# Kernel optimization log

Hardware: AMD Instinct MI355X
Metric: run time of the kernel (lower is better)

## Reference

```python
import jax, jax.numpy as jnp
import numpy as np

SL = 10   # seq_len hard-coded in rearrange
H = 20    # hidden size hard-coded in nn.LSTM
I = 128   # input_size
B = 32768 # batch


def setup_inputs() -> dict:
    key = jax.random.key(0)
    ks = jax.random.split(key, 9)
    k = 1.0 / np.sqrt(H)  # PyTorch LSTM init range
    u = lambda kk, shp: jax.random.uniform(kk, shp, jnp.float32, -k, k)
    return {
        "x": jax.random.normal(ks[0], (B * SL, I), jnp.float32),
        # gate order (PyTorch): i, f, g, o stacked along first dim (4H)
        "W_ih_f": u(ks[1], (4 * H, I)),
        "W_hh_f": u(ks[2], (4 * H, H)),
        "b_ih_f": u(ks[3], (4 * H,)),
        "b_hh_f": u(ks[4], (4 * H,)),
        "W_ih_b": u(ks[5], (4 * H, I)),
        "W_hh_b": u(ks[6], (4 * H, H)),
        "b_ih_b": u(ks[7], (4 * H,)),
        "b_hh_b": u(ks[8], (4 * H,)),
    }


def _lstm_scan(xp, W_hh):
    # xp: [T, B, 4H] precomputed input projection (+biases); returns hs [T, B, H]
    Bn = xp.shape[1]
    h0 = jnp.zeros((Bn, H), xp.dtype)
    c0 = jnp.zeros((Bn, H), xp.dtype)

    def step(carry, xt):
        h, c = carry
        g = xt + h @ W_hh.T
        i, f, gg, o = jnp.split(g, 4, axis=-1)
        i = jax.nn.sigmoid(i)
        f = jax.nn.sigmoid(f)
        gg = jnp.tanh(gg)
        o = jax.nn.sigmoid(o)
        c = f * c + i * gg
        h = o * jnp.tanh(c)
        return (h, c), h

    _, hs = jax.lax.scan(step, (h0, c0), xp)
    return hs


def reference(x, W_ih_f, W_hh_f, b_ih_f, b_hh_f, W_ih_b, W_hh_b, b_ih_b, b_hh_b):
    xb = x.reshape(-1, SL, I)  # '(b sl) i -> b sl i', sl=10
    # forward direction
    xp_f = jnp.einsum('bti,gi->tbg', xb, W_ih_f) + b_ih_f + b_hh_f
    hs_f = _lstm_scan(xp_f, W_hh_f)                     # [T,B,H]
    # backward direction: process reversed sequence
    xp_b = jnp.einsum('bti,gi->tbg', xb[:, ::-1], W_ih_b) + b_ih_b + b_hh_b
    hs_b = _lstm_scan(xp_b, W_hh_b)                     # [T,B,H] (reversed time order)
    # out = lstm_out[:, -1, :] : fwd hidden at t=SL-1 is hs_f[-1];
    # bwd hidden at original t=SL-1 is the FIRST reverse step, hs_b[0].
    return jnp.concatenate([hs_f[-1], hs_b[0]], axis=-1)  # [B, 2H]
```

## Files before the change

### kernel.cpp

```cpp
#include <hip/hip_runtime.h>

#define SL 10
#define NI 128

typedef float f32x4 __attribute__((ext_vector_type(4)));
typedef unsigned int u32;
typedef u32 u32x4 __attribute__((ext_vector_type(4)));
typedef __bf16 bfrag __attribute__((ext_vector_type(8)));

__device__ __forceinline__ u32 fb(float f){ return __float_as_uint(f); }
__device__ __forceinline__ float hi32(float f){ return __uint_as_float(fb(f)&0xFFFF0000u); }

__device__ __forceinline__ f32x4 MF(bfrag a, bfrag b, f32x4 c){
  return __builtin_amdgcn_mfma_f32_16x16x32_bf16(a, b, c, 0, 0, 0);
}

__device__ __forceinline__ float sigf(float x){ return __fdividef(1.f, 1.f + __expf(-x)); }
__device__ __forceinline__ float tanhf2(float x){ return __fdividef(2.f, 1.f + __expf(-2.f*x)) - 1.f; }

__device__ __forceinline__ void pack8(float4 a, float4 b, u32x4& hi, u32x4& lo){
  float f[8] = {a.x,a.y,a.z,a.w,b.x,b.y,b.z,b.w};
  #pragma unroll
  for(int j=0;j<4;j++){
    float p=f[2*j], q=f[2*j+1];
    hi[j] = (fb(p)>>16) | (fb(q)&0xFFFF0000u);
    float pr = p - hi32(p), qr = q - hi32(q);
    lo[j] = (fb(pr)>>16) | (fb(qr)&0xFFFF0000u);
  }
}
__device__ __forceinline__ void pack8hi(float4 a, float4 b, u32x4& hi){
  float f[8] = {a.x,a.y,a.z,a.w,b.x,b.y,b.z,b.w};
  #pragma unroll
  for(int j=0;j<4;j++)
    hi[j] = (fb(f[2*j])>>16) | (fb(f[2*j+1])&0xFFFF0000u);
}

__global__ __launch_bounds__(256, 2) void bilstm_kernel(
    const float* __restrict__ x,
    const float* __restrict__ Wih_f, const float* __restrict__ Whh_f,
    const float* __restrict__ bih_f, const float* __restrict__ bhh_f,
    const float* __restrict__ Wih_b,
    const float* __restrict__ bih_b, const float* __restrict__ bhh_b,
    float* __restrict__ out)
{
  __shared__ __attribute__((aligned(16))) u32 smem[16128];

  unsigned short* XH = (unsigned short*)smem;
  unsigned short* XL = XH + 64*136;
  u32*            WLp = smem + 8704;
  u32*            HB  = smem + 13824;

  const int tid  = threadIdx.x;
  const int lane = tid & 63;
  const int w    = tid >> 6;
  const int lr   = lane & 15;
  const int lg   = lane >> 4;
  const int b0   = blockIdx.x << 6;
  const int srow = tid >> 2;
  const int sseg = tid & 3;
  const int gbase = (lr&3)*20 + (lr>>2);

  for(int i=tid;i<64*36;i+=256) HB[i]=0;

  bfrag WHF[20];
  #pragma unroll
  for(int p=0;p<20;p++){
    const int nt=p>>2, ks=p&3;
    const float* src = Wih_f + (gbase + nt*4)*NI + ks*32 + lg*8;
    float4 a = *(const float4*)src;
    float4 b = *(const float4*)(src+4);
    u32x4 hi, lo;
    pack8(a,b,hi,lo);
    WHF[p] = __builtin_bit_cast(bfrag, hi);
    if(w == (p&3)) *(u32x4*)(WLp + p*256 + lane*4) = lo;
  }

  bfrag W2H[5], W2L[5];
  #pragma unroll
  for(int nt=0;nt<5;nt++){
    u32x4 hi, lo;
    #pragma unroll
    for(int j=0;j<4;j++){
      const int k0 = lg*8 + 2*j;
      float p = (k0   < 20) ? Whh_f[(gbase+nt*4)*20 + k0  ] : 0.f;
      float q = (k0+1 < 20) ? Whh_f[(gbase+nt*4)*20 + k0+1] : 0.f;
      hi[j] = (fb(p)>>16) | (fb(q)&0xFFFF0000u);
      float pr = p - hi32(p), qr = q - hi32(q);
      lo[j] = (fb(pr)>>16) | (fb(qr)&0xFFFF0000u);
    }
    W2H[nt] = __builtin_bit_cast(bfrag, hi);
    W2L[nt] = __builtin_bit_cast(bfrag, lo);
  }

  f32x4 biasv[5];
  #pragma unroll
  for(int nt=0;nt<5;nt++){
    const int u = nt*4+lg;
    f32x4 v;
    #pragma unroll
    for(int ty=0;ty<4;ty++) v[ty] = bih_f[ty*20+u] + bhh_f[ty*20+u];
    biasv[nt]=v;
  }

  float4 xs[8];
  {
    const float* p = x + ((long)(b0+srow)*SL)*NI + sseg*32;
    #pragma unroll
    for(int i=0;i<8;i++) xs[i] = ((const float4*)p)[i];
  }

  float cst[5] = {0.f,0.f,0.f,0.f,0.f};
  f32x4 acc[5];

  __syncthreads();

  for(int t=0;t<SL;t++){
    {
      unsigned short* dh = XH + srow*136 + sseg*32;
      unsigned short* dl = XL + srow*136 + sseg*32;
      #pragma unroll
      for(int c=0;c<4;c++){
        u32x4 hi, lo;
        pack8(xs[2*c], xs[2*c+1], hi, lo);
        *(u32x4*)(dh + c*8) = hi;
        *(u32x4*)(dl + c*8) = lo;
      }
    }
    __syncthreads();

    if(t+1<SL){
      const float* p = x + ((long)(b0+srow)*SL + (t+1))*NI + sseg*32;
      #pragma unroll
      for(int i=0;i<8;i++) xs[i] = ((const float4*)p)[i];
    }

    u32x4 h0, h1;
    if(t>0){
      const u32* hp = HB + (w*16+lr)*36 + lg*8;
      h0 = *(const u32x4*)hp;
      h1 = *(const u32x4*)(hp+4);
    }

    #pragma unroll
    for(int nt=0;nt<5;nt++) acc[nt] = biasv[nt];

    {
      const unsigned short* xrh = XH + (w*16+lr)*136;
      const unsigned short* xrl = XL + (w*16+lr)*136;
      #pragma unroll
      for(int ks=0;ks<4;ks++){
        bfrag bxh = *(const bfrag*)(xrh + ks*32 + lg*8);
        bfrag bxl = *(const bfrag*)(xrl + ks*32 + lg*8);
        #pragma unroll
        for(int nt=0;nt<5;nt++){
          const int p = nt*4+ks;
          bfrag wl = *(const bfrag*)(WLp + p*256 + lane*4);
          acc[nt] = MF(WHF[p], bxh, acc[nt]);
          acc[nt] = MF(wl,     bxh, acc[nt]);
          acc[nt] = MF(WHF[p], bxl, acc[nt]);
        }
      }
    }

    if(t>0){
      u32x4 hh, hl;
      hh[0] = (h0[0]>>16) | (h0[1]&0xFFFF0000u);
      hh[1] = (h0[2]>>16) | (h0[3]&0xFFFF0000u);
      hh[2] = (h1[0]>>16) | (h1[1]&0xFFFF0000u);
      hh[3] = (h1[2]>>16) | (h1[3]&0xFFFF0000u);
      hl[0] = (h0[0]&0xFFFFu) | (h0[1]<<16);
      hl[1] = (h0[2]&0xFFFFu) | (h0[3]<<16);
      hl[2] = (h1[0]&0xFFFFu) | (h1[1]<<16);
      hl[3] = (h1[2]&0xFFFFu) | (h1[3]<<16);
      bfrag bhh = __builtin_bit_cast(bfrag, hh);
      bfrag bhl = __builtin_bit_cast(bfrag, hl);
      #pragma unroll
      for(int nt=0;nt<5;nt++){
        acc[nt] = MF(W2H[nt], bhh, acc[nt]);
        acc[nt] = MF(W2L[nt], bhh, acc[nt]);
        acc[nt] = MF(W2H[nt], bhl, acc[nt]);
      }
    }

    #pragma unroll
    for(int nt=0;nt<5;nt++){
      float ig = sigf(acc[nt][0]);
      float fg = sigf(acc[nt][1]);
      float gg = tanhf2(acc[nt][2]);
      float og = sigf(acc[nt][3]);
      cst[nt] = fg*cst[nt] + ig*gg;
      float hv = og * tanhf2(cst[nt]);
      if(t==SL-1){
        out[(long)(b0+w*16+lr)*40 + nt*4+lg] = hv;
      } else {
        u32 hh16 = fb(hv)>>16;
        float hlf = hv - hi32(hv);
        HB[(w*16+lr)*36 + nt*4+lg] = (hh16<<16) | (fb(hlf)>>16);
      }
    }
    __syncthreads();
  }

  #pragma unroll
  for(int q=0;q<5;q++){
    const int G = q*256 + tid;
    const int p = G>>6, l = G&63;
    const int m = l&15, lgq = l>>4;
    const int g = (m&3)*20 + (p>>2)*4 + (m>>2);
    const float* src = Wih_b + g*NI + (p&3)*32 + lgq*8;
    float4 a = *(const float4*)src;
    float4 b = *(const float4*)(src+4);
    u32x4 hi;
    pack8hi(a,b,hi);
    *(u32x4*)(WLp + p*256 + l*4) = hi;
  }
  __syncthreads();

  {
    f32x4 acc2[5];
    #pragma unroll
    for(int nt=0;nt<5;nt++){
      const int u = nt*4+lg;
      f32x4 v;
      #pragma unroll
      for(int ty=0;ty<4;ty++) v[ty] = bih_b[ty*20+u] + bhh_b[ty*20+u];
      acc2[nt]=v;
    }
    const unsigned short* xrh = XH + (w*16+lr)*136;
    const unsigned short* xrl = XL + (w*16+lr)*136;
    #pragma unroll
    for(int ks=0;ks<4;ks++){
      bfrag bxh = *(const bfrag*)(xrh + ks*32 + lg*8);
      bfrag bxl = *(const bfrag*)(xrl + ks*32 + lg*8);
      #pragma unroll
      for(int nt=0;nt<5;nt++){
        const int p = nt*4+ks;
        bfrag wb = *(const bfrag*)(WLp + p*256 + lane*4);
        acc2[nt] = MF(wb, bxh, acc2[nt]);
        acc2[nt] = MF(wb, bxl, acc2[nt]);
      }
    }
    #pragma unroll
    for(int nt=0;nt<5;nt++){
      float ig = sigf(acc2[nt][0]);
      float gg = tanhf2(acc2[nt][2]);
      float og = sigf(acc2[nt][3]);
      float cb = ig*gg;
      out[(long)(b0+w*16+lr)*40 + 20 + nt*4+lg] = og * tanhf2(cb);
    }
  }
}

extern "C" void kernel_launch(void* const* d_in, const int* in_sizes, int n_in,
                              void* d_out, int out_size, void* d_ws, size_t ws_size,
                              hipStream_t stream) {
  const float* x     = (const float*)d_in[0];
  const float* Wih_f = (const float*)d_in[1];
  const float* Whh_f = (const float*)d_in[2];
  const float* bih_f = (const float*)d_in[3];
  const float* bhh_f = (const float*)d_in[4];
  const float* Wih_b = (const float*)d_in[5];
  const float* bih_b = (const float*)d_in[7];
  const float* bhh_b = (const float*)d_in[8];
  float* out = (float*)d_out;
  bilstm_kernel<<<dim3(512), dim3(256), 0, stream>>>(
      x, Wih_f, Whh_f, bih_f, bhh_f, Wih_b, bih_b, bhh_b, out);
}
```

Baseline: 63.60 us.

## Rewrite BiLSTM kernel with single-wave fp16 MFMA and register-resident inputs

Replaces the split-bf16 (hi/lo, three-MFMA) input projection with a single fp16 MFMA per tile, and keeps a two-term fp16 split only for the recurrent hidden state. Blocks shrink from four waves to one wave covering 16 rows, with x fed straight from registers rather than staged through LDS, which removes most __syncthreads and LDS traffic. The backward-direction weights are loaded from global memory directly into MFMA operands instead of being repacked in shared memory. This cuts MFMA count and synchronization, at the cost of reduced input precision (fp16 range/rounding on x and W_ih) and a smaller per-block working set that may lower wave occupancy per CU.

Result: faster. 52.64 us (-17.2%).

```diff
diff --git a/kernel.cpp b/kernel.cpp
--- a/kernel.cpp
+++ b/kernel.cpp
@@ -6,36 +6,22 @@
 typedef float f32x4 __attribute__((ext_vector_type(4)));
 typedef unsigned int u32;
 typedef u32 u32x4 __attribute__((ext_vector_type(4)));
-typedef __bf16 bfrag __attribute__((ext_vector_type(8)));
+typedef _Float16 h8 __attribute__((ext_vector_type(8)));
 
-__device__ __forceinline__ u32 fb(float f){ return __float_as_uint(f); }
-__device__ __forceinline__ float hi32(float f){ return __uint_as_float(fb(f)&0xFFFF0000u); }
-
-__device__ __forceinline__ f32x4 MF(bfrag a, bfrag b, f32x4 c){
-  return __builtin_amdgcn_mfma_f32_16x16x32_bf16(a, b, c, 0, 0, 0);
+__device__ __forceinline__ f32x4 MFH(h8 a, h8 b, f32x4 c){
+  return __builtin_amdgcn_mfma_f32_16x16x32_f16(a, b, c, 0, 0, 0);
 }
-
 __device__ __forceinline__ float sigf(float x){ return __fdividef(1.f, 1.f + __expf(-x)); }
 __device__ __forceinline__ float tanhf2(float x){ return __fdividef(2.f, 1.f + __expf(-2.f*x)) - 1.f; }
 
-__device__ __forceinline__ void pack8(float4 a, float4 b, u32x4& hi, u32x4& lo){
-  float f[8] = {a.x,a.y,a.z,a.w,b.x,b.y,b.z,b.w};
-  #pragma unroll
-  for(int j=0;j<4;j++){
-    float p=f[2*j], q=f[2*j+1];
-    hi[j] = (fb(p)>>16) | (fb(q)&0xFFFF0000u);
-    float pr = p - hi32(p), qr = q - hi32(q);
-    lo[j] = (fb(pr)>>16) | (fb(qr)&0xFFFF0000u);
-  }
-}
-__device__ __forceinline__ void pack8hi(float4 a, float4 b, u32x4& hi){
-  float f[8] = {a.x,a.y,a.z,a.w,b.x,b.y,b.z,b.w};
-  #pragma unroll
-  for(int j=0;j<4;j++)
-    hi[j] = (fb(f[2*j])>>16) | (fb(f[2*j+1])&0xFFFF0000u);
+__device__ __forceinline__ h8 to_h8(float4 a, float4 b){
+  h8 r;
+  r[0]=(_Float16)a.x; r[1]=(_Float16)a.y; r[2]=(_Float16)a.z; r[3]=(_Float16)a.w;
+  r[4]=(_Float16)b.x; r[5]=(_Float16)b.y; r[6]=(_Float16)b.z; r[7]=(_Float16)b.w;
+  return r;
 }
 
-__global__ __launch_bounds__(256, 2) void bilstm_kernel(
+__global__ __launch_bounds__(64, 2) void bilstm_kernel(
     const float* __restrict__ x,
     const float* __restrict__ Wih_f, const float* __restrict__ Whh_f,
     const float* __restrict__ bih_f, const float* __restrict__ bhh_f,
@@ -43,211 +29,131 @@
     const float* __restrict__ bih_b, const float* __restrict__ bhh_b,
     float* __restrict__ out)
 {
-  __shared__ __attribute__((aligned(16))) u32 smem[16128];
+  __shared__ u32 HB[16*33];
+  const int lane = threadIdx.x;
+  const int lr = lane & 15;
+  const int lg = lane >> 4;
+  const long row = (long)blockIdx.x*16 + lr;
+  const int gb = (lr&3)*20 + (lr>>2);
 
-  unsigned short* XH = (unsigned short*)smem;
-  unsigned short* XL = XH + 64*136;
-  u32*            WLp = smem + 8704;
-  u32*            HB  = smem + 13824;
+  for(int i=lane;i<16*33;i+=64) HB[i]=0;
 
-  const int tid  = threadIdx.x;
-  const int lane = tid & 63;
-  const int w    = tid >> 6;
-  const int lr   = lane & 15;
-  const int lg   = lane >> 4;
-  const int b0   = blockIdx.x << 6;
-  const int srow = tid >> 2;
-  const int sseg = tid & 3;
-  const int gbase = (lr&3)*20 + (lr>>2);
-
-  for(int i=tid;i<64*36;i+=256) HB[i]=0;
-
-  bfrag WHF[20];
+  h8 WIH[20];
   #pragma unroll
   for(int p=0;p<20;p++){
     const int nt=p>>2, ks=p&3;
-    const float* src = Wih_f + (gbase + nt*4)*NI + ks*32 + lg*8;
-    float4 a = *(const float4*)src;
-    float4 b = *(const float4*)(src+4);
-    u32x4 hi, lo;
-    pack8(a,b,hi,lo);
-    WHF[p] = __builtin_bit_cast(bfrag, hi);
-    if(w == (p&3)) *(u32x4*)(WLp + p*256 + lane*4) = lo;
+    const float* s = Wih_f + (gb+nt*4)*NI + ks*32 + lg*8;
+    WIH[p] = to_h8(*(const float4*)s, *(const float4*)(s+4));
+  }
+  h8 WHH[5];
+  #pragma unroll
+  for(int nt=0;nt<5;nt++){
+    h8 r;
+    #pragma unroll
+    for(int j=0;j<8;j++){
+      const int k = lg*8+j;
+      r[j] = (_Float16)((k<20) ? Whh_f[(gb+nt*4)*20+k] : 0.f);
+    }
+    WHH[nt]=r;
+  }
+  f32x4 biasv[5];
+  #pragma unroll
+  for(int nt=0;nt<5;nt++)
+    #pragma unroll
+    for(int ty=0;ty<4;ty++)
+      biasv[nt][ty] = bih_f[ty*20+nt*4+lg] + bhh_f[ty*20+nt*4+lg];
+
+  const float* xbase = x + row*(SL*NI) + lg*8;
+  float4 xa[4], xb4[4];
+  #pragma unroll
+  for(int ks=0;ks<4;ks++){
+    xa[ks]  = *(const float4*)(xbase + ks*32);
+    xb4[ks] = *(const float4*)(xbase + ks*32 + 4);
   }
 
-  bfrag W2H[5], W2L[5];
-  #pragma unroll
-  for(int nt=0;nt<5;nt++){
-    u32x4 hi, lo;
-    #pragma unroll
-    for(int j=0;j<4;j++){
-      const int k0 = lg*8 + 2*j;
-      float p = (k0   < 20) ? Whh_f[(gbase+nt*4)*20 + k0  ] : 0.f;
-      float q = (k0+1 < 20) ? Whh_f[(gbase+nt*4)*20 + k0+1] : 0.f;
-      hi[j] = (fb(p)>>16) | (fb(q)&0xFFFF0000u);
-      float pr = p - hi32(p), qr = q - hi32(q);
-      lo[j] = (fb(pr)>>16) | (fb(qr)&0xFFFF0000u);
-    }
-    W2H[nt] = __builtin_bit_cast(bfrag, hi);
-    W2L[nt] = __builtin_bit_cast(bfrag, lo);
-  }
-
-  f32x4 biasv[5];
-  #pragma unroll
-  for(int nt=0;nt<5;nt++){
-    const int u = nt*4+lg;
-    f32x4 v;
-    #pragma unroll
-    for(int ty=0;ty<4;ty++) v[ty] = bih_f[ty*20+u] + bhh_f[ty*20+u];
-    biasv[nt]=v;
-  }
-
-  float4 xs[8];
-  {
-    const float* p = x + ((long)(b0+srow)*SL)*NI + sseg*32;
-    #pragma unroll
-    for(int i=0;i<8;i++) xs[i] = ((const float4*)p)[i];
-  }
-
-  float cst[5] = {0.f,0.f,0.f,0.f,0.f};
+  float cst[5]={0.f,0.f,0.f,0.f,0.f};
+  h8 bx[4];
   f32x4 acc[5];
 
-  __syncthreads();
-
+  #pragma unroll
   for(int t=0;t<SL;t++){
-    {
-      unsigned short* dh = XH + srow*136 + sseg*32;
-      unsigned short* dl = XL + srow*136 + sseg*32;
+    #pragma unroll
+    for(int ks=0;ks<4;ks++) bx[ks]=to_h8(xa[ks],xb4[ks]);
+    if(t+1<SL){
       #pragma unroll
-      for(int c=0;c<4;c++){
-        u32x4 hi, lo;
-        pack8(xs[2*c], xs[2*c+1], hi, lo);
-        *(u32x4*)(dh + c*8) = hi;
-        *(u32x4*)(dl + c*8) = lo;
+      for(int ks=0;ks<4;ks++){
+        xa[ks]  = *(const float4*)(xbase + (t+1)*NI + ks*32);
+        xb4[ks] = *(const float4*)(xbase + (t+1)*NI + ks*32 + 4);
       }
     }
-    __syncthreads();
-
-    if(t+1<SL){
-      const float* p = x + ((long)(b0+srow)*SL + (t+1))*NI + sseg*32;
+    u32x4 hb0, hb1;
+    if(t>0){
+      const u32* hp = HB + lr*33 + lg*8;
+      hb0=*(const u32x4*)hp; hb1=*(const u32x4*)(hp+4);
+    }
+    #pragma unroll
+    for(int nt=0;nt<5;nt++) acc[nt]=biasv[nt];
+    #pragma unroll
+    for(int ks=0;ks<4;ks++)
       #pragma unroll
-      for(int i=0;i<8;i++) xs[i] = ((const float4*)p)[i];
-    }
-
-    u32x4 h0, h1;
-    if(t>0){
-      const u32* hp = HB + (w*16+lr)*36 + lg*8;
-      h0 = *(const u32x4*)hp;
-      h1 = *(const u32x4*)(hp+4);
-    }
-
-    #pragma unroll
-    for(int nt=0;nt<5;nt++) acc[nt] = biasv[nt];
-
-    {
-      const unsigned short* xrh = XH + (w*16+lr)*136;
-      const unsigned short* xrl = XL + (w*16+lr)*136;
-      #pragma unroll
-      for(int ks=0;ks<4;ks++){
-        bfrag bxh = *(const bfrag*)(xrh + ks*32 + lg*8);
-        bfrag bxl = *(const bfrag*)(xrl + ks*32 + lg*8);
-        #pragma unroll
-        for(int nt=0;nt<5;nt++){
-          const int p = nt*4+ks;
-          bfrag wl = *(const bfrag*)(WLp + p*256 + lane*4);
-          acc[nt] = MF(WHF[p], bxh, acc[nt]);
-          acc[nt] = MF(wl,     bxh, acc[nt]);
-          acc[nt] = MF(WHF[p], bxl, acc[nt]);
-        }
-      }
-    }
-
+      for(int nt=0;nt<5;nt++)
+        acc[nt]=MFH(WIH[nt*4+ks], bx[ks], acc[nt]);
     if(t>0){
       u32x4 hh, hl;
-      hh[0] = (h0[0]>>16) | (h0[1]&0xFFFF0000u);
-      hh[1] = (h0[2]>>16) | (h0[3]&0xFFFF0000u);
-      hh[2] = (h1[0]>>16) | (h1[1]&0xFFFF0000u);
-      hh[3] = (h1[2]>>16) | (h1[3]&0xFFFF0000u);
-      hl[0] = (h0[0]&0xFFFFu) | (h0[1]<<16);
-      hl[1] = (h0[2]&0xFFFFu) | (h0[3]<<16);
-      hl[2] = (h1[0]&0xFFFFu) | (h1[1]<<16);
-      hl[3] = (h1[2]&0xFFFFu) | (h1[3]<<16);
-      bfrag bhh = __builtin_bit_cast(bfrag, hh);
-      bfrag bhl = __builtin_bit_cast(bfrag, hl);
+      hh[0]=(hb0[0]>>16)|(hb0[1]&0xffff0000u);
+      hh[1]=(hb0[2]>>16)|(hb0[3]&0xffff0000u);
+      hh[2]=(hb1[0]>>16)|(hb1[1]&0xffff0000u);
+      hh[3]=(hb1[2]>>16)|(hb1[3]&0xffff0000u);
+      hl[0]=(hb0[0]&0xffffu)|(hb0[1]<<16);
+      hl[1]=(hb0[2]&0xffffu)|(hb0[3]<<16);
+      hl[2]=(hb1[0]&0xffffu)|(hb1[1]<<16);
+      hl[3]=(hb1[2]&0xffffu)|(hb1[3]<<16);
+      h8 fh=__builtin_bit_cast(h8,hh), fl=__builtin_bit_cast(h8,hl);
       #pragma unroll
       for(int nt=0;nt<5;nt++){
-        acc[nt] = MF(W2H[nt], bhh, acc[nt]);
-        acc[nt] = MF(W2L[nt], bhh, acc[nt]);
-        acc[nt] = MF(W2H[nt], bhl, acc[nt]);
-      }
-    }
-
-    #pragma unroll
-    for(int nt=0;nt<5;nt++){
-      float ig = sigf(acc[nt][0]);
-      float fg = sigf(acc[nt][1]);
-      float gg = tanhf2(acc[nt][2]);
-      float og = sigf(acc[nt][3]);
-      cst[nt] = fg*cst[nt] + ig*gg;
-      float hv = og * tanhf2(cst[nt]);
-      if(t==SL-1){
-        out[(long)(b0+w*16+lr)*40 + nt*4+lg] = hv;
-      } else {
-        u32 hh16 = fb(hv)>>16;
-        float hlf = hv - hi32(hv);
-        HB[(w*16+lr)*36 + nt*4+lg] = (hh16<<16) | (fb(hlf)>>16);
-      }
-    }
-    __syncthreads();
-  }
-
-  #pragma unroll
-  for(int q=0;q<5;q++){
-    const int G = q*256 + tid;
-    const int p = G>>6, l = G&63;
-    const int m = l&15, lgq = l>>4;
-    const int g = (m&3)*20 + (p>>2)*4 + (m>>2);
-    const float* src = Wih_b + g*NI + (p&3)*32 + lgq*8;
-    float4 a = *(const float4*)src;
-    float4 b = *(const float4*)(src+4);
-    u32x4 hi;
-    pack8hi(a,b,hi);
-    *(u32x4*)(WLp + p*256 + l*4) = hi;
-  }
-  __syncthreads();
-
-  {
-    f32x4 acc2[5];
-    #pragma unroll
-    for(int nt=0;nt<5;nt++){
-      const int u = nt*4+lg;
-      f32x4 v;
-      #pragma unroll
-      for(int ty=0;ty<4;ty++) v[ty] = bih_b[ty*20+u] + bhh_b[ty*20+u];
-      acc2[nt]=v;
-    }
-    const unsigned short* xrh = XH + (w*16+lr)*136;
-    const unsigned short* xrl = XL + (w*16+lr)*136;
-    #pragma unroll
-    for(int ks=0;ks<4;ks++){
-      bfrag bxh = *(const bfrag*)(xrh + ks*32 + lg*8);
-      bfrag bxl = *(const bfrag*)(xrl + ks*32 + lg*8);
-      #pragma unroll
-      for(int nt=0;nt<5;nt++){
-        const int p = nt*4+ks;
-        bfrag wb = *(const bfrag*)(WLp + p*256 + lane*4);
-        acc2[nt] = MF(wb, bxh, acc2[nt]);
-        acc2[nt] = MF(wb, bxl, acc2[nt]);
+        acc[nt]=MFH(WHH[nt], fh, acc[nt]);
+        acc[nt]=MFH(WHH[nt], fl, acc[nt]);
       }
     }
     #pragma unroll
     for(int nt=0;nt<5;nt++){
-      float ig = sigf(acc2[nt][0]);
-      float gg = tanhf2(acc2[nt][2]);
-      float og = sigf(acc2[nt][3]);
-      float cb = ig*gg;
-      out[(long)(b0+w*16+lr)*40 + 20 + nt*4+lg] = og * tanhf2(cb);
+      float ig=sigf(acc[nt][0]);
+      float fg=sigf(acc[nt][1]);
+      float gg=tanhf2(acc[nt][2]);
+      float og=sigf(acc[nt][3]);
+      cst[nt]=fg*cst[nt]+ig*gg;
+      float hv=og*tanhf2(cst[nt]);
+      if(t==SL-1){
+        out[row*40 + nt*4+lg] = hv;
+      } else {
+        _Float16 hh16=(_Float16)hv;
+        _Float16 hl16=(_Float16)(hv-(float)hh16);
+        HB[lr*33 + nt*4+lg] = ((u32)__builtin_bit_cast(unsigned short,hh16)<<16)
+                              | (u32)__builtin_bit_cast(unsigned short,hl16);
+      }
     }
+  }
+
+  f32x4 acc2[5];
+  #pragma unroll
+  for(int nt=0;nt<5;nt++)
+    #pragma unroll
+    for(int ty=0;ty<4;ty++)
+      acc2[nt][ty] = bih_b[ty*20+nt*4+lg] + bhh_b[ty*20+nt*4+lg];
+  #pragma unroll
+  for(int ks=0;ks<4;ks++){
+    #pragma unroll
+    for(int nt=0;nt<5;nt++){
+      const float* s = Wih_b + (gb+nt*4)*NI + ks*32 + lg*8;
+      acc2[nt]=MFH(to_h8(*(const float4*)s, *(const float4*)(s+4)), bx[ks], acc2[nt]);
+    }
+  }
+  #pragma unroll
+  for(int nt=0;nt<5;nt++){
+    float ig=sigf(acc2[nt][0]);
+    float gg=tanhf2(acc2[nt][2]);
+    float og=sigf(acc2[nt][3]);
+    out[row*40 + 20 + nt*4+lg] = og*tanhf2(ig*gg);
   }
 }
 
@@ -263,6 +169,6 @@
   const float* bih_b = (const float*)d_in[7];
   const float* bhh_b = (const float*)d_in[8];
   float* out = (float*)d_out;
-  bilstm_kernel<<<dim3(512), dim3(256), 0, stream>>>(
+  bilstm_kernel<<<dim3(2048), dim3(64), 0, stream>>>(
       x, Wih_f, Whh_f, bih_f, bhh_f, Wih_b, bih_b, bhh_b, out);
 }
```
